# Kernel tuning notes

Measured on AMD Instinct MI355X. Metric: run time of the kernel, lower is better.

The kernel has to match this reference:

```python
import jax, jax.numpy as jnp
import numpy as np

B, T, C = 1, 2048, 2048
N_HEAD, N_KV = 32, 8
HD = C // N_HEAD            # 64
N_REP = N_HEAD // N_KV      # 4
WINDOW = 512                # sliding_window
N_GLOBAL = 16               # n_global_tokens


def setup_inputs() -> dict:
    key = jax.random.key(0)
    ks = jax.random.split(key, 5)
    x = jax.random.normal(ks[0], (B, T, C), jnp.float32)
    # standard RoPE frequency tables, shape (T, HD//2)
    inv_freq = 1.0 / (10000.0 ** (np.arange(0, HD, 2, dtype=np.float32) / HD))
    ang = np.outer(np.arange(T, dtype=np.float32), inv_freq)
    freqs_cos = jnp.asarray(np.cos(ang), jnp.float32)
    freqs_sin = jnp.asarray(np.sin(ang), jnp.float32)
    s = 0.02
    wq = jax.random.normal(ks[1], (C, C), jnp.float32) * s
    wk = jax.random.normal(ks[2], (N_KV * HD, C), jnp.float32) * s
    wv = jax.random.normal(ks[3], (N_KV * HD, C), jnp.float32) * s
    wo = jax.random.normal(ks[4], (C, C), jnp.float32) * s
    return {"x": x, "freqs_cos": freqs_cos, "freqs_sin": freqs_sin,
            "wq": wq, "wk": wk, "wv": wv, "wo": wo}


def _apply_rope(xh, fc, fs):
    # xh: (B, H, T, HD); fc/fs: (T, HD//2) broadcast over (B, H)
    xr = xh.reshape(*xh.shape[:-1], HD // 2, 2)
    x0, x1 = xr[..., 0], xr[..., 1]
    fc = fc[None, None]
    fs = fs[None, None]
    out = jnp.stack([x0 * fc - x1 * fs, x0 * fs + x1 * fc], axis=-1)
    return out.reshape(xh.shape)


def reference(x, freqs_cos, freqs_sin, wq, wk, wv, wo):
    Bx, Tx, Cx = x.shape
    q = (x @ wq.T).reshape(Bx, Tx, N_HEAD, HD).transpose(0, 2, 1, 3)   # (B,Hq,T,hd)
    k = (x @ wk.T).reshape(Bx, Tx, N_KV, HD).transpose(0, 2, 1, 3)     # (B,Hkv,T,hd)
    v = (x @ wv.T).reshape(Bx, Tx, N_KV, HD).transpose(0, 2, 1, 3)
    q = _apply_rope(q, freqs_cos, freqs_sin)
    k = _apply_rope(k, freqs_cos, freqs_sin)

    # GQA: group query heads over shared kv heads instead of repeat_kv
    qg = q.reshape(Bx, N_KV, N_REP, Tx, HD)
    scale = 1.0 / float(np.sqrt(HD))
    scores = jnp.einsum('bgrqd,bgkd->bgrqk', qg, k) * scale  # (B,G,R,T,T)

    # sliding-window causal mask with global tokens (kv_cache=None branch)
    q_pos = jnp.arange(Tx)[:, None]
    k_pos = jnp.arange(Tx)[None, :]
    mask = (k_pos <= q_pos) & (k_pos >= q_pos - (WINDOW - 1))
    mask = mask | (k_pos < N_GLOBAL)
    # note: global columns combined with causal rows always leave >=1 valid key
    scores = jnp.where(mask[None, None, None], scores, -jnp.inf)
    probs = jax.nn.softmax(scores, axis=-1)

    y = jnp.einsum('bgrqk,bgkd->bgrqd', probs, v)
    y = y.reshape(Bx, N_HEAD, Tx, HD).transpose(0, 2, 1, 3).reshape(Bx, Tx, Cx)
    return y @ wo.T  # dropout p=0 in eval
```

## Files before the change

kernel.cpp:

```cpp
#include <hip/hip_runtime.h>
#include <hip/hip_bf16.h>

using short4v = __attribute__((ext_vector_type(4))) short;
using short8 = __attribute__((ext_vector_type(8))) short;
using f32x4  = __attribute__((ext_vector_type(4))) float;
using f32x16 = __attribute__((ext_vector_type(16))) float;
using int4v  = __attribute__((ext_vector_type(4))) int;

#define T_SEQ  2048
#define C_DIM  2048
#define NH     32
#define NKV    8
#define HD     64
#define WINDOW 512
#define NGLOB  16

__device__ inline ushort f2bf(float f) {
  union { float f; unsigned u; } v; v.f = f;
  unsigned u = v.u;
  u += 0x7fffu + ((u >> 16) & 1u);
  return (ushort)(u >> 16);
}
__device__ inline float bf2f(ushort h) {
  union { unsigned u; float f; } v; v.u = ((unsigned)h) << 16;
  return v.f;
}
__device__ inline float max3f(float a, float b, float c) { return fmaxf(fmaxf(a, b), c); }

__device__ __forceinline__ void gl_lds16(const ushort* g, ushort* l) {
  __builtin_amdgcn_global_load_lds(
      (const __attribute__((address_space(1))) void*)g,
      (__attribute__((address_space(3))) void*)l, 16, 0, 0);
}

__device__ __forceinline__ f32x16 zero16() {
  f32x16 v;
#pragma unroll
  for (int i = 0; i < 16; i++) v[i] = 0.f;
  return v;
}

__global__ void cvt_all(const float* __restrict__ s0, ushort* __restrict__ d0, int n0,
                        const float* __restrict__ s1, ushort* __restrict__ d1, int n1,
                        const float* __restrict__ s2, ushort* __restrict__ d2, int n2,
                        const float* __restrict__ s3, ushort* __restrict__ d3, int n3,
                        const float* __restrict__ s4, ushort* __restrict__ d4, int n4) {
  int total = n0 + n1 + n2 + n3 + n4;
  int stride = gridDim.x * blockDim.x;
  for (int i = blockIdx.x * blockDim.x + threadIdx.x; i < total; i += stride) {
    int j = i; const float* s; ushort* d;
    if (j < n0) { s = s0; d = d0; }
    else { j -= n0;
      if (j < n1) { s = s1; d = d1; }
      else { j -= n1;
        if (j < n2) { s = s2; d = d2; }
        else { j -= n2;
          if (j < n3) { s = s3; d = d3; }
          else { j -= n3; s = s4; d = d4; } } } }
    f32x4 a = *reinterpret_cast<const f32x4*>(s + (size_t)j * 8);
    f32x4 b = *reinterpret_cast<const f32x4*>(s + (size_t)j * 8 + 4);
    short8 o;
#pragma unroll
    for (int k = 0; k < 4; k++) { o[k] = (short)f2bf(a[k]); o[4 + k] = (short)f2bf(b[k]); }
    *reinterpret_cast<short8*>(d + (size_t)j * 8) = o;
  }
}

template <int MODE>
__global__ __launch_bounds__(512) void gemm2p(const ushort* __restrict__ A,
                                              const ushort* __restrict__ B0,
                                              const ushort* __restrict__ B1,
                                              const ushort* __restrict__ B2,
                                              void* __restrict__ C0,
                                              void* __restrict__ C1,
                                              void* __restrict__ C2,
                                              int K) {
  __shared__ ushort As[2][2][128][32];
  __shared__ ushort Bs[2][2][128][32];
  const int tid  = threadIdx.x;
  const int lane = tid & 63;
  const int wid  = tid >> 6;
  const int wr = wid >> 2, wc = wid & 3;
  const int r16 = lane & 15, g16 = (lane >> 4) & 3;
  const int bx = blockIdx.x, by = blockIdx.y;

  const ushort* Brow;
  void* Cout;
  int ldc, col0;
  bool vtr = false;
  if constexpr (MODE == 1) {
    if (bx < 16)      { Brow = B0 + (size_t)bx * 128 * K;        Cout = C0; ldc = 2048; col0 = bx * 128; }
    else if (bx < 20) { Brow = B1 + (size_t)(bx - 16) * 128 * K; Cout = C1; ldc = 512;  col0 = (bx - 16) * 128; }
    else              { Brow = B2 + (size_t)(bx - 20) * 128 * K; Cout = C2; ldc = 512;  col0 = (bx - 20) * 128; vtr = true; }
  } else {
    Brow = B0 + (size_t)bx * 128 * K; Cout = C0; ldc = 2048; col0 = bx * 128;
  }
  const ushort* Arow = A + (size_t)by * 128 * K;

  f32x4 acc[4][2];
#pragma unroll
  for (int i = 0; i < 4; i++)
#pragma unroll
    for (int j = 0; j < 2; j++) acc[i][j] = (f32x4){0.f, 0.f, 0.f, 0.f};

  const int srow = tid >> 2, scch = tid & 3;
  const int ssc  = scch ^ ((srow >> 1) & 3);
  const size_t agoff = (size_t)srow * K + ssc * 8;
  const int rchunk = (g16 ^ ((r16 >> 1) & 3)) * 8;

  const int nt = K >> 6;
  int d = 0;

#define STAGE(dd, k0)                                                         \
  {                                                                           \
    _Pragma("unroll") for (int kk = 0; kk < 2; kk++) {                        \
      gl_lds16(&Arow[agoff + (k0) + kk * 32], &As[dd][kk][srow][scch * 8]);   \
      gl_lds16(&Brow[agoff + (k0) + kk * 32], &Bs[dd][kk][srow][scch * 8]);   \
    }                                                                         \
  }

  STAGE(0, 0);
  __syncthreads();

  for (int t = 0; t < nt; ++t) {
    if (t + 1 < nt) STAGE(d ^ 1, (t + 1) * 64);
#pragma unroll
    for (int kk = 0; kk < 2; kk++) {
      short8 af[4], bfv[2];
#pragma unroll
      for (int i = 0; i < 4; i++)
        af[i] = *reinterpret_cast<const short8*>(&As[d][kk][wr * 64 + i * 16 + r16][rchunk]);
#pragma unroll
      for (int j = 0; j < 2; j++)
        bfv[j] = *reinterpret_cast<const short8*>(&Bs[d][kk][wc * 32 + j * 16 + r16][rchunk]);
#pragma unroll
      for (int i = 0; i < 4; i++)
#pragma unroll
        for (int j = 0; j < 2; j++)
          acc[i][j] = __builtin_amdgcn_mfma_f32_16x16x32_bf16(af[i], bfv[j], acc[i][j], 0, 0, 0);
    }
    __syncthreads();
    d ^= 1;
  }
#undef STAGE

#pragma unroll
  for (int i = 0; i < 4; i++)
#pragma unroll
    for (int j = 0; j < 2; j++) {
      int col = col0 + wc * 32 + j * 16 + r16;
      int row0 = by * 128 + wr * 64 + i * 16 + g16 * 4;
      if (MODE == 1 && vtr) {
        short4v tv;
#pragma unroll
        for (int r = 0; r < 4; r++) tv[r] = (short)f2bf(acc[i][j][r]);
        *reinterpret_cast<short4v*>(&((ushort*)Cout)[(size_t)col * T_SEQ + row0]) = tv;
      } else {
#pragma unroll
        for (int r = 0; r < 4; r++) {
          if constexpr (MODE == 0) ((float*)Cout)[(size_t)(row0 + r) * ldc + col] = acc[i][j][r];
          else                     ((ushort*)Cout)[(size_t)(row0 + r) * ldc + col] = f2bf(acc[i][j][r]);
        }
      }
    }
}

__global__ void rope2(ushort* __restrict__ Qb, ushort* __restrict__ Kb,
                      const float* __restrict__ fc, const float* __restrict__ fs) {
  int idx = blockIdx.x * blockDim.x + threadIdx.x;
  const int QN = T_SEQ * NH * 8;
  ushort* X; int t, hh, c, ld; float ksc;
  if (idx < QN) { X = Qb; c = idx & 7; hh = (idx >> 3) & 31; t = idx >> 8; ld = NH * HD;
                  ksc = 0.125f * 1.44269504089f; }
  else { idx -= QN; X = Kb; c = idx & 7; hh = (idx >> 3) & 7; t = idx >> 6; ld = NKV * HD;
         ksc = 1.0f; }
  size_t base = (size_t)t * ld + hh * HD + c * 8;
  short8 v = *reinterpret_cast<const short8*>(&X[base]);
  f32x4 cc = *reinterpret_cast<const f32x4*>(&fc[t * 32 + c * 4]);
  f32x4 ss = *reinterpret_cast<const f32x4*>(&fs[t * 32 + c * 4]);
  short8 o;
#pragma unroll
  for (int j = 0; j < 4; j++) {
    float x0 = bf2f((ushort)v[2 * j]), x1 = bf2f((ushort)v[2 * j + 1]);
    o[2 * j]     = (short)f2bf((x0 * cc[j] - x1 * ss[j]) * ksc);
    o[2 * j + 1] = (short)f2bf((x0 * ss[j] + x1 * cc[j]) * ksc);
  }
  *reinterpret_cast<short8*>(&X[base]) = o;
}

__global__ __launch_bounds__(512) void attn32(const ushort* __restrict__ Q,
                                              const ushort* __restrict__ K,
                                              const ushort* __restrict__ Vt,
                                              ushort* __restrict__ Y) {
  __shared__ float oS[4][64][33];
  __shared__ float mS[4][32];
  __shared__ float sS[4][64];
  ushort (*Ot)[32][72] = reinterpret_cast<ushort (*)[32][72]>(&oS[0][0][0]);
  const int lane = threadIdx.x & 63;
  const int wv   = threadIdx.x >> 6;
  const int hh   = wv & 3;
  const int split = wv >> 2;
  const int g  = blockIdx.x >> 6;
  const int qt = blockIdx.x & 63;
  const int h  = g * 4 + hh;
  const int q0 = qt << 5;
  const int l31 = lane & 31, hi = lane >> 5;
  const int hi8 = hi << 3, hi4 = hi << 2;
  const int qrow = q0 + l31;

  short8 qf[4];
#pragma unroll
  for (int s = 0; s < 4; s++)
    qf[s] = *reinterpret_cast<const short8*>(&Q[(size_t)qrow * C_DIM + h * HD + s * 16 + hi8]);

  f32x16 o[2] = { zero16(), zero16() };
  f32x16 sacc = zero16();
  float mrow = -1e30f;
  short8 ones8;
#pragma unroll
  for (int s = 0; s < 8; s++) ones8[s] = (short)0x3F80;

  auto pack8 = [&](const float* pp) -> short8 {
    unsigned wA, wB, wC, wD;
    asm("v_cvt_pk_bf16_f32 %0, %1, %2" : "=v"(wA) : "v"(pp[0]), "v"(pp[1]));
    asm("v_cvt_pk_bf16_f32 %0, %1, %2" : "=v"(wB) : "v"(pp[2]), "v"(pp[3]));
    asm("v_cvt_pk_bf16_f32 %0, %1, %2" : "=v"(wC) : "v"(pp[4]), "v"(pp[5]));
    asm("v_cvt_pk_bf16_f32 %0, %1, %2" : "=v"(wD) : "v"(pp[6]), "v"(pp[7]));
    asm("v_permlane32_swap_b32 %0, %1" : "+v"(wA), "+v"(wC));
    asm("v_permlane32_swap_b32 %0, %1" : "+v"(wB), "+v"(wD));
    int4v w4 = { (int)wA, (int)wB, (int)wC, (int)wD };
    return __builtin_bit_cast(short8, w4);
  };

#define LOADKV(kreg, vreg, kb)                                                     \
  {                                                                                \
    _Pragma("unroll") for (int s = 0; s < 4; s++)                                  \
      kreg[s] = *reinterpret_cast<const short8*>(                                  \
          &K[(size_t)((kb) + l31) * (NKV * HD) + g * HD + s * 16 + hi8]);          \
    _Pragma("unroll") for (int ntl = 0; ntl < 2; ntl++) {                          \
      const ushort* vp = &Vt[(size_t)(g * HD + ntl * 32 + l31) * T_SEQ + (kb) + hi8]; \
      vreg[2 * ntl]     = *reinterpret_cast<const short8*>(vp);                    \
      vreg[2 * ntl + 1] = *reinterpret_cast<const short8*>(vp + 16);               \
    }                                                                              \
  }

#define PROCESS(kreg, vreg, kb, domask)                                            \
  {                                                                                \
    f32x16 sa = zero16();                                                          \
    __builtin_amdgcn_s_setprio(1);                                                 \
    _Pragma("unroll") for (int s = 0; s < 4; s++)                                  \
      sa = __builtin_amdgcn_mfma_f32_32x32x16_bf16(kreg[s], qf[s], sa, 0, 0, 0);   \
    __builtin_amdgcn_s_setprio(0);                                                 \
    float p[16];                                                                   \
    _Pragma("unroll") for (int r = 0; r < 16; r++) p[r] = sa[r];                   \
    if (domask) {                                                                  \
      _Pragma("unroll") for (int r = 0; r < 16; r++) {                             \
        int kidx = (kb) + (r & 3) + 8 * (r >> 2) + hi4;                            \
        bool ok = ((kidx <= qrow) && (kidx >= qrow - (WINDOW - 1))) || (kidx < NGLOB); \
        p[r] = ok ? p[r] : -1e30f;                                                 \
      }                                                                            \
    }                                                                              \
    float m0 = max3f(p[0], p[1], p[2]);                                            \
    float m1 = max3f(p[3], p[4], p[5]);                                            \
    float m2 = max3f(p[6], p[7], p[8]);                                            \
    float m3 = max3f(p[9], p[10], p[11]);                                          \
    float m4 = max3f(p[12], p[13], p[14]);                                         \
    float tmax = fmaxf(max3f(m0, m1, m2), max3f(m3, m4, p[15]));                   \
    float pmax = fmaxf(tmax, __shfl_xor(tmax, 32));                                \
    if (!__all(pmax <= mrow + 8.0f)) {                                             \
      float mnew = fmaxf(mrow, pmax);                                              \
      float corr = exp2f(mrow - mnew);                                             \
      sacc[0] *= corr;                                                             \
      _Pragma("unroll") for (int r = 0; r < 16; r++) { o[0][r] *= corr; o[1][r] *= corr; } \
      mrow = mnew;                                                                 \
    }                                                                              \
    _Pragma("unroll") for (int r = 0; r < 16; r++) p[r] = exp2f(p[r] - mrow);      \
    short8 pb0 = pack8(&p[0]);                                                     \
    short8 pb1 = pack8(&p[8]);                                                     \
    __builtin_amdgcn_s_setprio(1);                                                 \
    sacc = __builtin_amdgcn_mfma_f32_32x32x16_bf16(ones8, pb0, sacc, 0, 0, 0);     \
    sacc = __builtin_amdgcn_mfma_f32_32x32x16_bf16(ones8, pb1, sacc, 0, 0, 0);     \
    o[0] = __builtin_amdgcn_mfma_f32_32x32x16_bf16(vreg[0], pb0, o[0], 0, 0, 0);   \
    o[0] = __builtin_amdgcn_mfma_f32_32x32x16_bf16(vreg[1], pb1, o[0], 0, 0, 0);   \
    o[1] = __builtin_amdgcn_mfma_f32_32x32x16_bf16(vreg[2], pb0, o[1], 0, 0, 0);   \
    o[1] = __builtin_amdgcn_mfma_f32_32x32x16_bf16(vreg[3], pb1, o[1], 0, 0, 0);   \
    __builtin_amdgcn_s_setprio(0);                                                 \
  }

  int wsr = (q0 - (WINDOW - 1)) >> 5;
  int wstart = (wsr < 1) ? 32 : (wsr << 5);
  int ntw = (q0 >= wstart) ? (((q0 - wstart) >> 5) + 1) : 0;
  const int NT = 1 + ntw;
  const int ihalf = (NT + 1) >> 1;
  const int i0 = split ? ihalf : 0;
  const int i1 = split ? NT : ihalf;

#define KBOF(i) ((i) == 0 ? 0 : wstart + ((i) - 1) * 32)
#define MSK(i)  ((i) == 0 || (KBOF(i) < q0 - 480) || (KBOF(i) == q0))

  short8 kA[4], vA[4], kB[4], vB[4];
  if (i0 < i1) {
    LOADKV(kA, vA, KBOF(i0));
    for (int i = i0; i < i1; i += 2) {
      if (i + 1 < i1) LOADKV(kB, vB, KBOF(i + 1));
      PROCESS(kA, vA, KBOF(i), MSK(i));
      if (i + 1 < i1) {
        if (i + 2 < i1) LOADKV(kA, vA, KBOF(i + 2));
        PROCESS(kB, vB, KBOF(i + 1), MSK(i + 1));
      }
    }
  }
#undef LOADKV
#undef PROCESS
#undef KBOF
#undef MSK

  float ssum = sacc[0];

  if (split == 1) {
    if (hi == 0) mS[hh][l31] = mrow;
    sS[hh][lane] = ssum;
#pragma unroll
    for (int ntl = 0; ntl < 2; ntl++)
#pragma unroll
      for (int r = 0; r < 16; r++) oS[hh][lane][ntl * 16 + r] = o[ntl][r];
  }
  __syncthreads();

  float inv = 0.f;
  if (split == 0) {
    float mB = mS[hh][l31];
    float sB = sS[hh][lane];
    float mN = fmaxf(mrow, mB);
    float cA = exp2f(mrow - mN), cB = exp2f(mB - mN);
    ssum = ssum * cA + sB * cB;
#pragma unroll
    for (int ntl = 0; ntl < 2; ntl++)
#pragma unroll
      for (int r = 0; r < 16; r++)
        o[ntl][r] = o[ntl][r] * cA + oS[hh][lane][ntl * 16 + r] * cB;
    inv = 1.0f / ssum;
  }
  __syncthreads();

  if (split == 0) {
#pragma unroll
    for (int ntl = 0; ntl < 2; ntl++)
#pragma unroll
      for (int r = 0; r < 16; r++) {
        int dim = ntl * 32 + (r & 3) + 8 * (r >> 2) + hi4;
        Ot[hh][l31][dim] = f2bf(o[ntl][r] * inv);
      }
  }
  __syncthreads();

  if (split == 0) {
    int qq = lane >> 1, hf = lane & 1;
#pragma unroll
    for (int c = 0; c < 4; c++) {
      short8 vv = *reinterpret_cast<const short8*>(&Ot[hh][qq][hf * 32 + c * 8]);
      *reinterpret_cast<short8*>(&Y[(size_t)(q0 + qq) * C_DIM + h * HD + hf * 32 + c * 8]) = vv;
    }
  }
}

extern "C" void kernel_launch(void* const* d_in, const int* in_sizes, int n_in,
                              void* d_out, int out_size, void* d_ws, size_t ws_size,
                              hipStream_t stream) {
  const float* x  = (const float*)d_in[0];
  const float* fc = (const float*)d_in[1];
  const float* fs = (const float*)d_in[2];
  const float* wq = (const float*)d_in[3];
  const float* wk = (const float*)d_in[4];
  const float* wv = (const float*)d_in[5];
  const float* wo = (const float*)d_in[6];
  float* out = (float*)d_out;

  const size_t SZ_X = (size_t)T_SEQ * C_DIM;
  const size_t SZ_W = (size_t)(NKV * HD) * C_DIM;

  ushort* xb  = (ushort*)d_ws;
  ushort* wqb = xb  + SZ_X;
  ushort* wkb = wqb + SZ_X;
  ushort* wvb = wkb + SZ_W;
  ushort* wob = wvb + SZ_W;
  ushort* Qb  = wob + SZ_X;
  ushort* Kb  = Qb  + SZ_X;
  ushort* Vt  = Kb  + SZ_W;
  ushort* Yb  = Vt  + SZ_W;

  cvt_all<<<1024, 256, 0, stream>>>(x,  xb,  (int)(SZ_X / 8),
                                    wq, wqb, (int)(SZ_X / 8),
                                    wk, wkb, (int)(SZ_W / 8),
                                    wv, wvb, (int)(SZ_W / 8),
                                    wo, wob, (int)(SZ_X / 8));

  gemm2p<1><<<dim3(24, 16), 512, 0, stream>>>(xb, wqb, wkb, wvb, Qb, Kb, Vt, C_DIM);

  rope2<<<(T_SEQ * (NH + NKV) * 8) / 256, 256, 0, stream>>>(Qb, Kb, fc, fs);

  attn32<<<512, 512, 0, stream>>>(Qb, Kb, Vt, Yb);

  gemm2p<0><<<dim3(16, 16), 512, 0, stream>>>(Yb, wob, nullptr, nullptr, out, nullptr, nullptr, C_DIM);
}
```

Baseline: 138.5 us.

## Stage K/V tiles through swizzled LDS with double buffering shared across heads

Replaces per-wave direct global loads of K and V fragments with cooperative global-to-LDS loads (gl_lds16) into XOR-swizzled, double-buffered shared tiles. The four query heads in a GQA group then read the same staged tile from LDS. This cuts redundant global/L2 traffic, since previously each of the 4 head waves loaded identical K/V. The block index mapping is also changed to interleave KV groups and process the last query tiles first, which should help load balance. The cost is extra LDS use and a block-wide barrier every iteration, which couples the two split halves.

```diff
diff --git a/kernel.cpp b/kernel.cpp
--- a/kernel.cpp
+++ b/kernel.cpp
@@ -192,16 +192,19 @@
                                               const ushort* __restrict__ K,
                                               const ushort* __restrict__ Vt,
                                               ushort* __restrict__ Y) {
+  __shared__ ushort Klds[2][2][2048];
+  __shared__ ushort Vlds[2][2][2048];
   __shared__ float oS[4][64][33];
   __shared__ float mS[4][32];
   __shared__ float sS[4][64];
   ushort (*Ot)[32][72] = reinterpret_cast<ushort (*)[32][72]>(&oS[0][0][0]);
-  const int lane = threadIdx.x & 63;
-  const int wv   = threadIdx.x >> 6;
+  const int tid  = threadIdx.x;
+  const int lane = tid & 63;
+  const int wv   = tid >> 6;
   const int hh   = wv & 3;
   const int split = wv >> 2;
-  const int g  = blockIdx.x >> 6;
-  const int qt = blockIdx.x & 63;
+  const int g  = blockIdx.x & 7;
+  const int qt = 63 - (blockIdx.x >> 3);
   const int h  = g * 4 + hh;
   const int q0 = qt << 5;
   const int l31 = lane & 31, hi = lane >> 5;
@@ -232,24 +235,48 @@
     return __builtin_bit_cast(short8, w4);
   };
 
-#define LOADKV(kreg, vreg, kb)                                                     \
+  int wsr = (q0 - (WINDOW - 1)) >> 5;
+  int wstart = (wsr < 1) ? 32 : (wsr << 5);
+  int ntw = (q0 >= wstart) ? (((q0 - wstart) >> 5) + 1) : 0;
+  const int NT = 1 + ntw;
+  const int ihalf = (NT + 1) >> 1;
+
+#define KBOF(i) ((i) == 0 ? 0 : wstart + ((i) - 1) * 32)
+#define MSK(i)  ((i) == 0 || (KBOF(i) < q0 - 480) || (KBOF(i) == q0))
+
+  const int sp_s = tid >> 8;
+  const int kr = (tid >> 3) & 31, kc = tid & 7;
+  const int vr = (tid >> 2) & 63, vc = tid & 3;
+  const ushort* ksrc0 = K + (size_t)kr * (NKV * HD) + g * HD + ((kc ^ (kr & 7)) * 8);
+  const ushort* vsrc0 = Vt + (size_t)(g * HD + vr) * T_SEQ + ((vc ^ ((vr >> 1) & 3)) * 8);
+  ushort* kdst[2] = { &Klds[sp_s][0][(tid & 255) * 8], &Klds[sp_s][1][(tid & 255) * 8] };
+  ushort* vdst[2] = { &Vlds[sp_s][0][(tid & 255) * 8], &Vlds[sp_s][1][(tid & 255) * 8] };
+
+#define STAGE(dd, i0t, i1t)                                                    \
+  {                                                                            \
+    int idxs = sp_s ? (i1t) : (i0t);                                           \
+    if (idxs > NT - 1) idxs = NT - 1;                                          \
+    int kbs = KBOF(idxs);                                                      \
+    gl_lds16(ksrc0 + (size_t)kbs * (NKV * HD), kdst[dd]);                      \
+    gl_lds16(vsrc0 + kbs, vdst[dd]);                                           \
+  }
+
+#define PROCESS(dd, kb, domask)                                                    \
   {                                                                                \
-    _Pragma("unroll") for (int s = 0; s < 4; s++)                                  \
-      kreg[s] = *reinterpret_cast<const short8*>(                                  \
-          &K[(size_t)((kb) + l31) * (NKV * HD) + g * HD + s * 16 + hi8]);          \
-    _Pragma("unroll") for (int ntl = 0; ntl < 2; ntl++) {                          \
-      const ushort* vp = &Vt[(size_t)(g * HD + ntl * 32 + l31) * T_SEQ + (kb) + hi8]; \
-      vreg[2 * ntl]     = *reinterpret_cast<const short8*>(vp);                    \
-      vreg[2 * ntl + 1] = *reinterpret_cast<const short8*>(vp + 16);               \
-    }                                                                              \
-  }
-
-#define PROCESS(kreg, vreg, kb, domask)                                            \
-  {                                                                                \
+    short8 kf0 = *reinterpret_cast<const short8*>(                                 \
+        &Klds[split][dd][l31 * 64 + (((0 * 2 + hi) ^ (l31 & 7)) * 8)]);            \
+    short8 kf1 = *reinterpret_cast<const short8*>(                                 \
+        &Klds[split][dd][l31 * 64 + (((1 * 2 + hi) ^ (l31 & 7)) * 8)]);            \
+    short8 kf2 = *reinterpret_cast<const short8*>(                                 \
+        &Klds[split][dd][l31 * 64 + (((2 * 2 + hi) ^ (l31 & 7)) * 8)]);            \
+    short8 kf3 = *reinterpret_cast<const short8*>(                                 \
+        &Klds[split][dd][l31 * 64 + (((3 * 2 + hi) ^ (l31 & 7)) * 8)]);            \
     f32x16 sa = zero16();                                                          \
     __builtin_amdgcn_s_setprio(1);                                                 \
-    _Pragma("unroll") for (int s = 0; s < 4; s++)                                  \
-      sa = __builtin_amdgcn_mfma_f32_32x32x16_bf16(kreg[s], qf[s], sa, 0, 0, 0);   \
+    sa = __builtin_amdgcn_mfma_f32_32x32x16_bf16(kf0, qf[0], sa, 0, 0, 0);         \
+    sa = __builtin_amdgcn_mfma_f32_32x32x16_bf16(kf1, qf[1], sa, 0, 0, 0);         \
+    sa = __builtin_amdgcn_mfma_f32_32x32x16_bf16(kf2, qf[2], sa, 0, 0, 0);         \
+    sa = __builtin_amdgcn_mfma_f32_32x32x16_bf16(kf3, qf[3], sa, 0, 0, 0);         \
     __builtin_amdgcn_s_setprio(0);                                                 \
     float p[16];                                                                   \
     _Pragma("unroll") for (int r = 0; r < 16; r++) p[r] = sa[r];                   \
@@ -277,40 +304,38 @@
     _Pragma("unroll") for (int r = 0; r < 16; r++) p[r] = exp2f(p[r] - mrow);      \
     short8 pb0 = pack8(&p[0]);                                                     \
     short8 pb1 = pack8(&p[8]);                                                     \
+    short8 v0 = *reinterpret_cast<const short8*>(                                  \
+        &Vlds[split][dd][(0 * 32 + l31) * 32 + (((0 * 2 + hi) ^ ((l31 >> 1) & 3)) * 8)]); \
+    short8 v1 = *reinterpret_cast<const short8*>(                                  \
+        &Vlds[split][dd][(0 * 32 + l31) * 32 + (((1 * 2 + hi) ^ ((l31 >> 1) & 3)) * 8)]); \
+    short8 v2 = *reinterpret_cast<const short8*>(                                  \
+        &Vlds[split][dd][(1 * 32 + l31) * 32 + (((0 * 2 + hi) ^ (((32 + l31) >> 1) & 3)) * 8)]); \
+    short8 v3 = *reinterpret_cast<const short8*>(                                  \
+        &Vlds[split][dd][(1 * 32 + l31) * 32 + (((1 * 2 + hi) ^ (((32 + l31) >> 1) & 3)) * 8)]); \
     __builtin_amdgcn_s_setprio(1);                                                 \
     sacc = __builtin_amdgcn_mfma_f32_32x32x16_bf16(ones8, pb0, sacc, 0, 0, 0);     \
     sacc = __builtin_amdgcn_mfma_f32_32x32x16_bf16(ones8, pb1, sacc, 0, 0, 0);     \
-    o[0] = __builtin_amdgcn_mfma_f32_32x32x16_bf16(vreg[0], pb0, o[0], 0, 0, 0);   \
-    o[0] = __builtin_amdgcn_mfma_f32_32x32x16_bf16(vreg[1], pb1, o[0], 0, 0, 0);   \
-    o[1] = __builtin_amdgcn_mfma_f32_32x32x16_bf16(vreg[2], pb0, o[1], 0, 0, 0);   \
-    o[1] = __builtin_amdgcn_mfma_f32_32x32x16_bf16(vreg[3], pb1, o[1], 0, 0, 0);   \
+    o[0] = __builtin_amdgcn_mfma_f32_32x32x16_bf16(v0, pb0, o[0], 0, 0, 0);        \
+    o[0] = __builtin_amdgcn_mfma_f32_32x32x16_bf16(v1, pb1, o[0], 0, 0, 0);        \
+    o[1] = __builtin_amdgcn_mfma_f32_32x32x16_bf16(v2, pb0, o[1], 0, 0, 0);        \
+    o[1] = __builtin_amdgcn_mfma_f32_32x32x16_bf16(v3, pb1, o[1], 0, 0, 0);        \
     __builtin_amdgcn_s_setprio(0);                                                 \
   }
 
-  int wsr = (q0 - (WINDOW - 1)) >> 5;
-  int wstart = (wsr < 1) ? 32 : (wsr << 5);
-  int ntw = (q0 >= wstart) ? (((q0 - wstart) >> 5) + 1) : 0;
-  const int NT = 1 + ntw;
-  const int ihalf = (NT + 1) >> 1;
-  const int i0 = split ? ihalf : 0;
-  const int i1 = split ? NT : ihalf;
-
-#define KBOF(i) ((i) == 0 ? 0 : wstart + ((i) - 1) * 32)
-#define MSK(i)  ((i) == 0 || (KBOF(i) < q0 - 480) || (KBOF(i) == q0))
-
-  short8 kA[4], vA[4], kB[4], vB[4];
-  if (i0 < i1) {
-    LOADKV(kA, vA, KBOF(i0));
-    for (int i = i0; i < i1; i += 2) {
-      if (i + 1 < i1) LOADKV(kB, vB, KBOF(i + 1));
-      PROCESS(kA, vA, KBOF(i), MSK(i));
-      if (i + 1 < i1) {
-        if (i + 2 < i1) LOADKV(kA, vA, KBOF(i + 2));
-        PROCESS(kB, vB, KBOF(i + 1), MSK(i + 1));
-      }
+  STAGE(0, 0, ihalf);
+  __syncthreads();
+  int d = 0;
+  for (int it = 0; it < ihalf; ++it) {
+    if (it + 1 < ihalf) STAGE(d ^ 1, it + 1, ihalf + it + 1);
+    int idx = split ? (ihalf + it) : it;
+    if (idx < NT) {
+      int kb = KBOF(idx);
+      PROCESS(d, kb, MSK(idx));
     }
-  }
-#undef LOADKV
+    __syncthreads();
+    d ^= 1;
+  }
+#undef STAGE
 #undef PROCESS
 #undef KBOF
 #undef MSK
```

Measured after the change: 123.7 us. 10.7% less time.
